# Optimization experiments

Measured on AMD Instinct MI355X. Metric: run time of the kernel, lower is better.

Reference implementation:

```python
import jax, jax.numpy as jnp
import numpy as np

N_NODES = 21
HID = 32


def _gcn_norm(edge_index, n):
    # GCNConv normalization with added self-loops (improved=False)
    src, dst = edge_index[0], edge_index[1]
    loop = jnp.arange(n, dtype=src.dtype)
    s = jnp.concatenate([src, loop])
    d = jnp.concatenate([dst, loop])
    w = jnp.ones(s.shape[0], dtype=jnp.float32)
    deg = jnp.zeros(n, dtype=jnp.float32).at[d].add(w)
    dinv = jnp.where(deg > 0, deg ** -0.5, 0.0)
    return s, d, dinv[s] * w * dinv[d]


def _gcn(X, W, b, s, d, norm):
    # X: [B,P,N,F] -> [B,P,N,O]; gather along node axis, scatter-add at targets
    XW = X @ W
    msg = XW[:, :, s, :] * norm[None, None, :, None]
    out = jnp.zeros_like(XW[:, :, :1, :]).repeat(XW.shape[2], axis=2)
    out = jnp.zeros(XW.shape, XW.dtype).at[:, :, d, :].add(msg)
    return out + b


def _forward(x, edge_index, W_z, b_z, W_r, b_r, W_h, b_h,
             lz_W, lz_b, lr_W, lr_b, lh_W, lh_b,
             att, l1_W, l1_b, l2_W, l2_b):
    B, N, F, P = x.shape
    X = jnp.transpose(x, (0, 3, 1, 2))  # [B,P,N,F] -- all periods in parallel
    s, d, norm = _gcn_norm(edge_index, N)
    # A3TGCN2 passes H=None for every period -> hidden state is zeros each call
    H = jnp.zeros((B, P, N, HID), x.dtype)
    Z = jax.nn.sigmoid(jnp.concatenate([_gcn(X, W_z, b_z, s, d, norm), H], -1) @ lz_W + lz_b)
    R = jax.nn.sigmoid(jnp.concatenate([_gcn(X, W_r, b_r, s, d, norm), H], -1) @ lr_W + lr_b)
    Ht = jnp.tanh(jnp.concatenate([_gcn(X, W_h, b_h, s, d, norm), H * R], -1) @ lh_W + lh_b)
    Hn = Z * H + (1.0 - Z) * Ht  # [B,P,N,HID]
    probs = jax.nn.softmax(att)
    h = jnp.einsum('p,bpno->bno', probs, Hn)  # attention pooling over periods
    h = jax.nn.relu(h)
    h = h @ l1_W + l1_b            # [B,N,P]
    h = jnp.transpose(h, (0, 2, 1))  # [B,P,N]
    h = h @ l2_W + l2_b            # [B,P,6]
    return jnp.transpose(h, (0, 2, 1))  # [B,6,P]


def setup_inputs() -> dict:
    key = jax.random.key(0)
    ks = jax.random.split(key, 16)
    B, N, F, P = 1024, N_NODES, 3, 64
    x = jax.random.normal(ks[0], (B, N, F, P), jnp.float32)
    edge_index = jax.random.randint(ks[1], (2, 60), 0, N)
    sc = 0.1
    inp = {
        'x': x, 'edge_index': edge_index,
        'W_z': jax.random.normal(ks[2], (F, HID)) * sc, 'b_z': jnp.zeros(HID),
        'W_r': jax.random.normal(ks[3], (F, HID)) * sc, 'b_r': jnp.zeros(HID),
        'W_h': jax.random.normal(ks[4], (F, HID)) * sc, 'b_h': jnp.zeros(HID),
        'lz_W': jax.random.normal(ks[5], (2 * HID, HID)) * sc, 'lz_b': jnp.zeros(HID),
        'lr_W': jax.random.normal(ks[6], (2 * HID, HID)) * sc, 'lr_b': jnp.zeros(HID),
        'lh_W': jax.random.normal(ks[7], (2 * HID, HID)) * sc, 'lh_b': jnp.zeros(HID),
        'att': jax.random.uniform(ks[8], (P,)),
        'l1_W': jax.random.normal(ks[9], (HID, P)) * sc, 'l1_b': jnp.zeros(P),
        'l2_W': jax.random.normal(ks[10], (N, 6)) * sc, 'l2_b': jnp.zeros(6),
    }
    return inp


def reference(x, edge_index, W_z, b_z, W_r, b_r, W_h, b_h,
              lz_W, lz_b, lr_W, lr_b, lh_W, lh_b,
              att, l1_W, l1_b, l2_W, l2_b):
    return _forward(x, edge_index, W_z, b_z, W_r, b_r, W_h, b_h,
                    lz_W, lz_b, lr_W, lr_b, lh_W, lh_b,
                    att, l1_W, l1_b, l2_W, l2_b)
```

## Files before the change

### kernel.cpp

```cpp
#include <hip/hip_runtime.h>

#define NN   21
#define NE   60
#define FD   3
#define HD   32
#define PP   64
#define OUTC 6
#define LOG2E 1.44269504088896f

#define WS_A    0
#define WS_WZ   504
#define WS_WH   600
#define WS_BZ   696
#define WS_BH   728
#define WS_PROB 760
#define WS_M    824

#if defined(__has_builtin)
#  if __has_builtin(__builtin_amdgcn_exp2f)
#    define EXP2(x) __builtin_amdgcn_exp2f(x)
#  else
#    define EXP2(x) exp2f(x)
#  endif
#else
#  define EXP2(x) exp2f(x)
#endif
#define RCP(x) __builtin_amdgcn_rcpf(x)

__global__ void setup_k(const int* __restrict__ edge,
                        const float* __restrict__ Wz, const float* __restrict__ bz,
                        const float* __restrict__ Wh, const float* __restrict__ bh,
                        const float* __restrict__ lzW, const float* __restrict__ lzb,
                        const float* __restrict__ lhW, const float* __restrict__ lhb,
                        const float* __restrict__ att, const float* __restrict__ l1b,
                        const float* __restrict__ l2W, const float* __restrict__ l2b,
                        float* __restrict__ ws) {
    __shared__ float sA[NN * NN];
    __shared__ float degS[NN];
    __shared__ float ScS[OUTC];
    const int t = threadIdx.x;

    for (int i = t; i < NN * NN; i += 256) sA[i] = 0.f;
    if (t < NN) degS[t] = 1.f;
    __syncthreads();

    if (t < NE) atomicAdd(&degS[edge[NE + t]], 1.f);
    __syncthreads();

    if (t < NN) degS[t] = rsqrtf(degS[t]);
    __syncthreads();

    if (t < NE) {
        int s = edge[t], d = edge[NE + t];
        atomicAdd(&sA[d * NN + s], degS[s] * degS[d]);
    }
    if (t >= 64 && t < 64 + NN) {
        int n = t - 64;
        atomicAdd(&sA[n * NN + n], degS[n] * degS[n]);
    }
    if (t >= 96 && t < 192) {
        int i = t - 96, f = i >> 5, o = i & 31;
        float az = 0.f, ah = 0.f;
        for (int k = 0; k < HD; ++k) {
            az = fmaf(Wz[f * HD + k], lzW[k * HD + o], az);
            ah = fmaf(Wh[f * HD + k], lhW[k * HD + o], ah);
        }
        ws[WS_WZ + i] = az * LOG2E;
        ws[WS_WH + i] = ah * (2.f * LOG2E);
    }
    if (t >= 192 && t < 224) {
        int o = t - 192;
        float az = lzb[o], ah = lhb[o];
        for (int k = 0; k < HD; ++k) {
            az = fmaf(bz[k], lzW[k * HD + o], az);
            ah = fmaf(bh[k], lhW[k * HD + o], ah);
        }
        ws[WS_BZ + o] = az * LOG2E;
        ws[WS_BH + o] = ah * (2.f * LOG2E);
    }
    if (t < 64) {
        float a = att[t], m = a;
        #pragma unroll
        for (int msk = 32; msk >= 1; msk >>= 1) m = fmaxf(m, __shfl_xor(m, msk, 64));
        float e = __expf(a - m);
        float ssum = e;
        #pragma unroll
        for (int msk = 32; msk >= 1; msk >>= 1) ssum += __shfl_xor(ssum, msk, 64);
        ws[WS_PROB + t] = e / ssum;
    }
    if (t >= 224 && t < 224 + OUTC) {
        int c = t - 224;
        float s = 0.f;
        for (int n = 0; n < NN; ++n) s += l2W[n * OUTC + c];
        ScS[c] = s;
    }
    __syncthreads();

    for (int i = t; i < NN * 24; i += 256) {
        int r = i / 24, cm = i % 24;
        ws[WS_A + i] = (cm < NN) ? sA[r * NN + cm] : 0.f;
    }
    for (int i = t; i < OUTC * PP; i += 256) {
        int c = i >> 6, p = i & 63;
        ws[WS_M + i] = fmaf(ScS[c], l1b[p], l2b[c]);
    }
}

#define EVAL(Y0,Y1,Y2,PR) do {                                                  \
    float az0_ = fmaf((Y2), wz02, fmaf((Y1), wz01, fmaf((Y0), wz00, bz0)));     \
    float ah0_ = fmaf((Y2), wh02, fmaf((Y1), wh01, fmaf((Y0), wh00, bh0)));     \
    float w0_  = RCP(1.f + EXP2(az0_));                                         \
    float h0_  = fmaf(-2.f, RCP(1.f + EXP2(ah0_)), 1.f);                        \
    acc0 = fmaf((PR) * w0_, h0_, acc0);                                         \
    float az1_ = fmaf((Y2), wz12, fmaf((Y1), wz11, fmaf((Y0), wz10, bz1)));     \
    float ah1_ = fmaf((Y2), wh12, fmaf((Y1), wh11, fmaf((Y0), wh10, bh1)));     \
    float w1_  = RCP(1.f + EXP2(az1_));                                         \
    float h1_  = fmaf(-2.f, RCP(1.f + EXP2(ah1_)), 1.f);                        \
    acc1 = fmaf((PR) * w1_, h1_, acc1);                                         \
} while (0)

__global__ __launch_bounds__(512, 8) void main_k(
    const float* __restrict__ x,  const float* __restrict__ ws,
    const float* __restrict__ l1W, const float* __restrict__ l2W,
    float* __restrict__ out)
{
    __shared__ __align__(16) float Xs[NN * FD * PP];
    __shared__ __align__(16) float Ys[NN * FD * PP];
    __shared__ __align__(16) float AsP[NN * 24];
    __shared__ __align__(16) float Cs[320];
    __shared__ float Hs[NN * HD];
    __shared__ float G[OUTC * HD];

    const int t = threadIdx.x;
    const int b = blockIdx.x;
    const float* xb = x + (size_t)b * (NN * FD * PP);

    {
        const float4* xb4 = (const float4*)xb;
        float4* Xs4 = (float4*)Xs;
        Xs4[t] = xb4[t];
        if (t < 496) Xs4[512 + t] = xb4[512 + t];
        if (t < 126) ((float4*)AsP)[t] = ((const float4*)ws)[t];
        if (t >= 128 && t < 208)
            ((float4*)Cs)[t - 128] = ((const float4*)(ws + WS_WZ))[t - 128];
    }
    __syncthreads();

    {
        const float4* Xs4 = (const float4*)Xs;
        float4* Ys4 = (float4*)Ys;
        for (int i = t; i < NN * FD * PP / 4; i += 512) {
            const int p4 = i & 15;
            const int fn = i >> 4;
            const int n  = fn / 3;
            const int f  = fn - n * 3;
            const float4* An4 = (const float4*)(AsP + n * 24);
            float4 acc = {0.f, 0.f, 0.f, 0.f};
            #pragma unroll
            for (int mq = 0; mq < 6; ++mq) {
                const float4 a = An4[mq];
                if (a.x != 0.f) { const float4 xv = Xs4[((mq*4+0)*3+f)*16 + p4];
                    acc.x=fmaf(a.x,xv.x,acc.x); acc.y=fmaf(a.x,xv.y,acc.y);
                    acc.z=fmaf(a.x,xv.z,acc.z); acc.w=fmaf(a.x,xv.w,acc.w); }
                if (a.y != 0.f) { const float4 xv = Xs4[((mq*4+1)*3+f)*16 + p4];
                    acc.x=fmaf(a.y,xv.x,acc.x); acc.y=fmaf(a.y,xv.y,acc.y);
                    acc.z=fmaf(a.y,xv.z,acc.z); acc.w=fmaf(a.y,xv.w,acc.w); }
                if (a.z != 0.f) { const float4 xv = Xs4[((mq*4+2)*3+f)*16 + p4];
                    acc.x=fmaf(a.z,xv.x,acc.x); acc.y=fmaf(a.z,xv.y,acc.y);
                    acc.z=fmaf(a.z,xv.z,acc.z); acc.w=fmaf(a.z,xv.w,acc.w); }
                if (a.w != 0.f) { const float4 xv = Xs4[((mq*4+3)*3+f)*16 + p4];
                    acc.x=fmaf(a.w,xv.x,acc.x); acc.y=fmaf(a.w,xv.y,acc.y);
                    acc.z=fmaf(a.w,xv.z,acc.z); acc.w=fmaf(a.w,xv.w,acc.w); }
            }
            Ys4[fn * 16 + p4] = acc;
        }
    }
    __syncthreads();

    {
        const int ps = t & 7;
        const int og = (t >> 3) & 15;
        const int c4 = t >> 7;
        const int o0 = og * 2, o1 = o0 + 1;
        const float wz00 = Cs[o0],      wz01 = Cs[32+o0],  wz02 = Cs[64+o0];
        const float wz10 = Cs[o1],      wz11 = Cs[32+o1],  wz12 = Cs[64+o1];
        const float wh00 = Cs[96+o0],   wh01 = Cs[128+o0], wh02 = Cs[160+o0];
        const float wh10 = Cs[96+o1],   wh11 = Cs[128+o1], wh12 = Cs[160+o1];
        const float bz0  = Cs[192+o0],  bz1  = Cs[192+o1];
        const float bh0  = Cs[224+o0],  bh1  = Cs[224+o1];
        const float4 pr0 = *(const float4*)&Cs[256 + ps*8];
        const float4 pr1 = *(const float4*)&Cs[256 + ps*8 + 4];
        #pragma unroll
        for (int s = 0; s < 6; ++s) {
            const int n = c4 + 4 * s;
            if (n < NN) {
                const float4* Yn4 = (const float4*)(Ys + n * FD * PP) + ps * 2;
                float acc0 = 0.f, acc1 = 0.f;
                float4 y0 = Yn4[0], y1 = Yn4[16], y2 = Yn4[32];
                EVAL(y0.x,y1.x,y2.x, pr0.x); EVAL(y0.y,y1.y,y2.y, pr0.y);
                EVAL(y0.z,y1.z,y2.z, pr0.z); EVAL(y0.w,y1.w,y2.w, pr0.w);
                y0 = Yn4[1]; y1 = Yn4[17]; y2 = Yn4[33];
                EVAL(y0.x,y1.x,y2.x, pr1.x); EVAL(y0.y,y1.y,y2.y, pr1.y);
                EVAL(y0.z,y1.z,y2.z, pr1.z); EVAL(y0.w,y1.w,y2.w, pr1.w);
                acc0 += __shfl_xor(acc0, 1); acc0 += __shfl_xor(acc0, 2); acc0 += __shfl_xor(acc0, 4);
                acc1 += __shfl_xor(acc1, 1); acc1 += __shfl_xor(acc1, 2); acc1 += __shfl_xor(acc1, 4);
                if (ps == 0) {
                    Hs[n * HD + o0] = fmaxf(acc0, 0.f);
                    Hs[n * HD + o1] = fmaxf(acc1, 0.f);
                }
            }
        }
    }
    __syncthreads();

    if (t < OUTC * HD) {
        const int c = t >> 5, o = t & 31;
        float g = 0.f;
        #pragma unroll
        for (int n = 0; n < NN; ++n)
            g = fmaf(l2W[n * OUTC + c], Hs[n * HD + o], g);
        G[t] = g;
    }
    __syncthreads();

    if (t < OUTC * PP) {
        const int c = t >> 6, p = t & 63;
        const float* Gc = G + c * HD;
        float a0 = 0.f, a1 = 0.f, a2 = 0.f, a3 = 0.f;
        #pragma unroll
        for (int o = 0; o < HD; o += 4) {
            a0 = fmaf(Gc[o+0], l1W[(o+0) * PP + p], a0);
            a1 = fmaf(Gc[o+1], l1W[(o+1) * PP + p], a1);
            a2 = fmaf(Gc[o+2], l1W[(o+2) * PP + p], a2);
            a3 = fmaf(Gc[o+3], l1W[(o+3) * PP + p], a3);
        }
        out[(size_t)b * (OUTC * PP) + t] = ws[WS_M + t] + (a0 + a1) + (a2 + a3);
    }
}

extern "C" void kernel_launch(void* const* d_in, const int* in_sizes, int n_in,
                              void* d_out, int out_size, void* d_ws, size_t ws_size,
                              hipStream_t stream) {
    const float* x   = (const float*)d_in[0];
    const int*   ei  = (const int*)  d_in[1];
    const float* Wz  = (const float*)d_in[2];
    const float* bz  = (const float*)d_in[3];
    const float* Wh  = (const float*)d_in[6];
    const float* bh  = (const float*)d_in[7];
    const float* lzW = (const float*)d_in[8];
    const float* lzb = (const float*)d_in[9];
    const float* lhW = (const float*)d_in[12];
    const float* lhb = (const float*)d_in[13];
    const float* att = (const float*)d_in[14];
    const float* l1W = (const float*)d_in[15];
    const float* l1b = (const float*)d_in[16];
    const float* l2W = (const float*)d_in[17];
    const float* l2b = (const float*)d_in[18];

    float* out = (float*)d_out;
    float* ws  = (float*)d_ws;

    const int B = in_sizes[0] / (NN * FD * PP);

    setup_k<<<1, 256, 0, stream>>>(ei, Wz, bz, Wh, bh, lzW, lzb, lhW, lhb,
                                   att, l1b, l2W, l2b, ws);
    main_k<<<B, 512, 0, stream>>>(x, ws, l1W, l2W, out);
}
```

Baseline: 128.3 us.

## Fuse setup kernel into main kernel and merge sigmoid-tanh reciprocals

Removes the separate single-block setup kernel and has every block recompute the normalized adjacency, folded gate weights, softmax probabilities and output bias in shared memory, which saves a launch and the serial dependency on it. The gate evaluation now combines the sigmoid and tanh reciprocals into a single reciprocal of a product. l1W is staged into shared memory, reusing the X buffer. The cost is redundant setup work in every one of the 1024 blocks, extra barriers, and possible overflow in the product of two exponentials for large pre-activations.

New measurement: 128.9 us, median of 2. About the same (+0.5%).

```diff
diff --git a/kernel.cpp b/kernel.cpp
--- a/kernel.cpp
+++ b/kernel.cpp
@@ -7,14 +7,6 @@
 #define PP   64
 #define OUTC 6
 #define LOG2E 1.44269504088896f
-
-#define WS_A    0
-#define WS_WZ   504
-#define WS_WH   600
-#define WS_BZ   696
-#define WS_BH   728
-#define WS_PROB 760
-#define WS_M    824
 
 #if defined(__has_builtin)
 #  if __has_builtin(__builtin_amdgcn_exp2f)
@@ -27,107 +19,34 @@
 #endif
 #define RCP(x) __builtin_amdgcn_rcpf(x)
 
-__global__ void setup_k(const int* __restrict__ edge,
-                        const float* __restrict__ Wz, const float* __restrict__ bz,
-                        const float* __restrict__ Wh, const float* __restrict__ bh,
-                        const float* __restrict__ lzW, const float* __restrict__ lzb,
-                        const float* __restrict__ lhW, const float* __restrict__ lhb,
-                        const float* __restrict__ att, const float* __restrict__ l1b,
-                        const float* __restrict__ l2W, const float* __restrict__ l2b,
-                        float* __restrict__ ws) {
-    __shared__ float sA[NN * NN];
-    __shared__ float degS[NN];
-    __shared__ float ScS[OUTC];
-    const int t = threadIdx.x;
-
-    for (int i = t; i < NN * NN; i += 256) sA[i] = 0.f;
-    if (t < NN) degS[t] = 1.f;
-    __syncthreads();
-
-    if (t < NE) atomicAdd(&degS[edge[NE + t]], 1.f);
-    __syncthreads();
-
-    if (t < NN) degS[t] = rsqrtf(degS[t]);
-    __syncthreads();
-
-    if (t < NE) {
-        int s = edge[t], d = edge[NE + t];
-        atomicAdd(&sA[d * NN + s], degS[s] * degS[d]);
-    }
-    if (t >= 64 && t < 64 + NN) {
-        int n = t - 64;
-        atomicAdd(&sA[n * NN + n], degS[n] * degS[n]);
-    }
-    if (t >= 96 && t < 192) {
-        int i = t - 96, f = i >> 5, o = i & 31;
-        float az = 0.f, ah = 0.f;
-        for (int k = 0; k < HD; ++k) {
-            az = fmaf(Wz[f * HD + k], lzW[k * HD + o], az);
-            ah = fmaf(Wh[f * HD + k], lhW[k * HD + o], ah);
-        }
-        ws[WS_WZ + i] = az * LOG2E;
-        ws[WS_WH + i] = ah * (2.f * LOG2E);
-    }
-    if (t >= 192 && t < 224) {
-        int o = t - 192;
-        float az = lzb[o], ah = lhb[o];
-        for (int k = 0; k < HD; ++k) {
-            az = fmaf(bz[k], lzW[k * HD + o], az);
-            ah = fmaf(bh[k], lhW[k * HD + o], ah);
-        }
-        ws[WS_BZ + o] = az * LOG2E;
-        ws[WS_BH + o] = ah * (2.f * LOG2E);
-    }
-    if (t < 64) {
-        float a = att[t], m = a;
-        #pragma unroll
-        for (int msk = 32; msk >= 1; msk >>= 1) m = fmaxf(m, __shfl_xor(m, msk, 64));
-        float e = __expf(a - m);
-        float ssum = e;
-        #pragma unroll
-        for (int msk = 32; msk >= 1; msk >>= 1) ssum += __shfl_xor(ssum, msk, 64);
-        ws[WS_PROB + t] = e / ssum;
-    }
-    if (t >= 224 && t < 224 + OUTC) {
-        int c = t - 224;
-        float s = 0.f;
-        for (int n = 0; n < NN; ++n) s += l2W[n * OUTC + c];
-        ScS[c] = s;
-    }
-    __syncthreads();
-
-    for (int i = t; i < NN * 24; i += 256) {
-        int r = i / 24, cm = i % 24;
-        ws[WS_A + i] = (cm < NN) ? sA[r * NN + cm] : 0.f;
-    }
-    for (int i = t; i < OUTC * PP; i += 256) {
-        int c = i >> 6, p = i & 63;
-        ws[WS_M + i] = fmaf(ScS[c], l1b[p], l2b[c]);
-    }
-}
-
 #define EVAL(Y0,Y1,Y2,PR) do {                                                  \
     float az0_ = fmaf((Y2), wz02, fmaf((Y1), wz01, fmaf((Y0), wz00, bz0)));     \
     float ah0_ = fmaf((Y2), wh02, fmaf((Y1), wh01, fmaf((Y0), wh00, bh0)));     \
-    float w0_  = RCP(1.f + EXP2(az0_));                                         \
-    float h0_  = fmaf(-2.f, RCP(1.f + EXP2(ah0_)), 1.f);                        \
-    acc0 = fmaf((PR) * w0_, h0_, acc0);                                         \
+    float ea0_ = EXP2(az0_), e20_ = EXP2(ah0_);                                 \
+    float r0_  = RCP((1.f + ea0_) * (1.f + e20_));                              \
+    acc0 = fmaf(fmaf((PR), e20_, -(PR)), r0_, acc0);                            \
     float az1_ = fmaf((Y2), wz12, fmaf((Y1), wz11, fmaf((Y0), wz10, bz1)));     \
     float ah1_ = fmaf((Y2), wh12, fmaf((Y1), wh11, fmaf((Y0), wh10, bh1)));     \
-    float w1_  = RCP(1.f + EXP2(az1_));                                         \
-    float h1_  = fmaf(-2.f, RCP(1.f + EXP2(ah1_)), 1.f);                        \
-    acc1 = fmaf((PR) * w1_, h1_, acc1);                                         \
+    float ea1_ = EXP2(az1_), e21_ = EXP2(ah1_);                                 \
+    float r1_  = RCP((1.f + ea1_) * (1.f + e21_));                              \
+    acc1 = fmaf(fmaf((PR), e21_, -(PR)), r1_, acc1);                            \
 } while (0)
 
-__global__ __launch_bounds__(512, 8) void main_k(
-    const float* __restrict__ x,  const float* __restrict__ ws,
-    const float* __restrict__ l1W, const float* __restrict__ l2W,
+__global__ __launch_bounds__(512, 8) void fused_k(
+    const float* __restrict__ x,   const int* __restrict__ edge,
+    const float* __restrict__ Wz,  const float* __restrict__ bz,
+    const float* __restrict__ Wh,  const float* __restrict__ bh,
+    const float* __restrict__ lzW, const float* __restrict__ lzb,
+    const float* __restrict__ lhW, const float* __restrict__ lhb,
+    const float* __restrict__ att,
+    const float* __restrict__ l1W, const float* __restrict__ l1b,
+    const float* __restrict__ l2W, const float* __restrict__ l2b,
     float* __restrict__ out)
 {
     __shared__ __align__(16) float Xs[NN * FD * PP];
     __shared__ __align__(16) float Ys[NN * FD * PP];
     __shared__ __align__(16) float AsP[NN * 24];
-    __shared__ __align__(16) float Cs[320];
+    __shared__ __align__(16) float Cs[352];
     __shared__ float Hs[NN * HD];
     __shared__ float G[OUTC * HD];
 
@@ -140,9 +59,57 @@
         float4* Xs4 = (float4*)Xs;
         Xs4[t] = xb4[t];
         if (t < 496) Xs4[512 + t] = xb4[512 + t];
-        if (t < 126) ((float4*)AsP)[t] = ((const float4*)ws)[t];
-        if (t >= 128 && t < 208)
-            ((float4*)Cs)[t - 128] = ((const float4*)(ws + WS_WZ))[t - 128];
+        for (int i = t; i < NN * 24; i += 512) AsP[i] = 0.f;
+        if (t < NN) Cs[320 + t] = 1.f;
+    }
+    __syncthreads();
+
+    if (t < NE) {
+        atomicAdd(&Cs[320 + edge[NE + t]], 1.f);
+    } else if (t >= 64 && t < 160) {
+        int i = t - 64, f = i >> 5, o = i & 31;
+        float az = 0.f, ah = 0.f;
+        #pragma unroll
+        for (int k = 0; k < HD; ++k) {
+            az = fmaf(Wz[f * HD + k], lzW[k * HD + o], az);
+            ah = fmaf(Wh[f * HD + k], lhW[k * HD + o], ah);
+        }
+        Cs[i] = az * LOG2E;
+        Cs[96 + i] = ah * (2.f * LOG2E);
+    } else if (t >= 160 && t < 192) {
+        int o = t - 160;
+        float az = lzb[o], ah = lhb[o];
+        #pragma unroll
+        for (int k = 0; k < HD; ++k) {
+            az = fmaf(bz[k], lzW[k * HD + o], az);
+            ah = fmaf(bh[k], lhW[k * HD + o], ah);
+        }
+        Cs[192 + o] = az * LOG2E;
+        Cs[224 + o] = ah * (2.f * LOG2E);
+    } else if (t >= 192 && t < 256) {
+        int l = t - 192;
+        float a = att[l], m = a;
+        #pragma unroll
+        for (int msk = 32; msk >= 1; msk >>= 1) m = fmaxf(m, __shfl_xor(m, msk, 64));
+        float e = __expf(a - m);
+        float ssum = e;
+        #pragma unroll
+        for (int msk = 32; msk >= 1; msk >>= 1) ssum += __shfl_xor(ssum, msk, 64);
+        Cs[256 + l] = e / ssum;
+    } else if (t >= 256 && t < 256 + OUTC) {
+        int c = t - 256;
+        float s = 0.f;
+        for (int n = 0; n < NN; ++n) s += l2W[n * OUTC + c];
+        Cs[344 + c] = s;
+    }
+    __syncthreads();
+
+    if (t < NE) {
+        int s = edge[t], d = edge[NE + t];
+        atomicAdd(&AsP[d * 24 + s], rsqrtf(Cs[320 + s]) * rsqrtf(Cs[320 + d]));
+    } else if (t >= 64 && t < 64 + NN) {
+        int n = t - 64;
+        atomicAdd(&AsP[n * 24 + n], RCP(Cs[320 + n]));
     }
     __syncthreads();
 
@@ -177,17 +144,19 @@
     }
     __syncthreads();
 
+    ((float4*)Xs)[t] = ((const float4*)l1W)[t];
+
     {
         const int ps = t & 7;
         const int og = (t >> 3) & 15;
         const int c4 = t >> 7;
         const int o0 = og * 2, o1 = o0 + 1;
-        const float wz00 = Cs[o0],      wz01 = Cs[32+o0],  wz02 = Cs[64+o0];
-        const float wz10 = Cs[o1],      wz11 = Cs[32+o1],  wz12 = Cs[64+o1];
-        const float wh00 = Cs[96+o0],   wh01 = Cs[128+o0], wh02 = Cs[160+o0];
-        const float wh10 = Cs[96+o1],   wh11 = Cs[128+o1], wh12 = Cs[160+o1];
-        const float bz0  = Cs[192+o0],  bz1  = Cs[192+o1];
-        const float bh0  = Cs[224+o0],  bh1  = Cs[224+o1];
+        const float wz00 = Cs[o0],     wz01 = Cs[32+o0],  wz02 = Cs[64+o0];
+        const float wz10 = Cs[o1],     wz11 = Cs[32+o1],  wz12 = Cs[64+o1];
+        const float wh00 = Cs[96+o0],  wh01 = Cs[128+o0], wh02 = Cs[160+o0];
+        const float wh10 = Cs[96+o1],  wh11 = Cs[128+o1], wh12 = Cs[160+o1];
+        const float bz0  = Cs[192+o0], bz1  = Cs[192+o1];
+        const float bh0  = Cs[224+o0], bh1  = Cs[224+o1];
         const float4 pr0 = *(const float4*)&Cs[256 + ps*8];
         const float4 pr1 = *(const float4*)&Cs[256 + ps*8 + 4];
         #pragma unroll
@@ -220,21 +189,27 @@
         for (int n = 0; n < NN; ++n)
             g = fmaf(l2W[n * OUTC + c], Hs[n * HD + o], g);
         G[t] = g;
+    } else {
+        for (int i = t - 192; i < OUTC * PP; i += 320) {
+            const int c = i >> 6, p = i & 63;
+            Ys[i] = fmaf(Cs[344 + c], l1b[p], l2b[c]);
+        }
     }
     __syncthreads();
 
     if (t < OUTC * PP) {
         const int c = t >> 6, p = t & 63;
         const float* Gc = G + c * HD;
+        const float* l1Ws = Xs;
         float a0 = 0.f, a1 = 0.f, a2 = 0.f, a3 = 0.f;
         #pragma unroll
         for (int o = 0; o < HD; o += 4) {
-            a0 = fmaf(Gc[o+0], l1W[(o+0) * PP + p], a0);
-            a1 = fmaf(Gc[o+1], l1W[(o+1) * PP + p], a1);
-            a2 = fmaf(Gc[o+2], l1W[(o+2) * PP + p], a2);
-            a3 = fmaf(Gc[o+3], l1W[(o+3) * PP + p], a3);
-        }
-        out[(size_t)b * (OUTC * PP) + t] = ws[WS_M + t] + (a0 + a1) + (a2 + a3);
+            a0 = fmaf(Gc[o+0], l1Ws[(o+0) * PP + p], a0);
+            a1 = fmaf(Gc[o+1], l1Ws[(o+1) * PP + p], a1);
+            a2 = fmaf(Gc[o+2], l1Ws[(o+2) * PP + p], a2);
+            a3 = fmaf(Gc[o+3], l1Ws[(o+3) * PP + p], a3);
+        }
+        out[(size_t)b * (OUTC * PP) + t] = Ys[t] + (a0 + a1) + (a2 + a3);
     }
 }
 
@@ -258,11 +233,8 @@
     const float* l2b = (const float*)d_in[18];
 
     float* out = (float*)d_out;
-    float* ws  = (float*)d_ws;
-
     const int B = in_sizes[0] / (NN * FD * PP);
 
-    setup_k<<<1, 256, 0, stream>>>(ei, Wz, bz, Wh, bh, lzW, lzb, lhW, lhb,
-                                   att, l1b, l2W, l2b, ws);
-    main_k<<<B, 512, 0, stream>>>(x, ws, l1W, l2W, out);
+    fused_k<<<B, 512, 0, stream>>>(x, ei, Wz, bz, Wh, bh, lzW, lzb, lhW, lhb,
+                                   att, l1W, l1b, l2W, l2b, out);
 }
```
